# Kernel tuning notes

Hardware: AMD Instinct MI355X
Metric: run time of the kernel (lower is better)

## Reference

```python
import jax, jax.numpy as jnp
import numpy as np

# DAG: node -> list of children; node 0 is the stem output, node 6 is the cell output.
GRAPH = {1: [0], 2: [0, 1], 3: [1, 2], 4: [2, 3], 5: [3, 4], 6: [4, 5]}
OUTPUT_NODE = 6


def conv3x3(x, w, b):
    # x: [N,C,H,W], w: [O,I,3,3], b: [O]; stride 1, SAME padding (PyTorch Conv2d pad=1)
    y = jax.lax.conv_general_dilated(
        x, w, window_strides=(1, 1), padding='SAME',
        dimension_numbers=('NCHW', 'OIHW', 'NCHW'))
    return y + b[None, :, None, None]


def setup_inputs() -> dict:
    key = jax.random.key(0)
    k_x, k_w0, k_b0, k_wn, k_bn = jax.random.split(key, 5)
    scale = 0.05  # keep activations bounded through 7 stacked convs
    return {
        'x': jax.random.normal(k_x, (8, 64, 64, 64), dtype=jnp.float32),
        'W0': jax.random.normal(k_w0, (128, 64, 3, 3), dtype=jnp.float32) * scale,
        'b0': jax.random.normal(k_b0, (128,), dtype=jnp.float32) * scale,
        'Wn': jax.random.normal(k_wn, (6, 128, 128, 3, 3), dtype=jnp.float32) * scale,
        'bn': jax.random.normal(k_bn, (6, 128), dtype=jnp.float32) * scale,
    }


def reference(x, W0, b0, Wn, bn):
    # activations[0] = layers['0'](x)
    acts = {0: conv3x3(x, W0, b0)}
    # DFS with memoization over a DAG == topological evaluation of nodes 1..6.
    # Each node n sums its OWN conv (weights Wn[n-1]) applied to every child activation.
    for node in range(1, OUTPUT_NODE + 1):
        w, b = Wn[node - 1], bn[node - 1]
        out = None
        for child in GRAPH[node]:
            y = conv3x3(acts[child], w, b)
            out = y if out is None else out + y
        acts[node] = out
    return acts[OUTPUT_NODE]
```

## Files before the change

### kernel.cpp

```cpp
#include <hip/hip_runtime.h>


typedef __bf16 bf16x8 __attribute__((ext_vector_type(8)));
typedef float f32x4 __attribute__((ext_vector_type(4)));

union U4 { uint4 u; bf16x8 b; };

__device__ inline unsigned pk_bf16(float lo, float hi) {
  unsigned r;
  asm volatile("v_cvt_pk_bf16_f32 %0, %1, %2" : "=v"(r) : "v"(lo), "v"(hi));
  return r;
}

__device__ inline unsigned addpk(unsigned a, unsigned b) {
  float alo = __builtin_bit_cast(float, a << 16);
  float ahi = __builtin_bit_cast(float, a & 0xFFFF0000u);
  float blo = __builtin_bit_cast(float, b << 16);
  float bhi = __builtin_bit_cast(float, b & 0xFFFF0000u);
  return pk_bf16(alo + blo, ahi + bhi);
}

__device__ inline uint4 addpk4(uint4 a, uint4 b) {
  return make_uint4(addpk(a.x, b.x), addpk(a.y, b.y), addpk(a.z, b.z), addpk(a.w, b.w));
}

__device__ __forceinline__ void gload16(const unsigned* g, unsigned* l) {
  __builtin_amdgcn_global_load_lds(
      (const __attribute__((address_space(1))) unsigned*)(g),
      (__attribute__((address_space(3))) unsigned*)(l), 16, 0, 0);
}

template <int N>
__device__ __forceinline__ void waitcnt_vm_lgkm() {
  if constexpr (N == 0)
    asm volatile("s_waitcnt vmcnt(0) lgkmcnt(0)" ::: "memory");
  else if constexpr (N == 1)
    asm volatile("s_waitcnt vmcnt(1) lgkmcnt(0)" ::: "memory");
  else
    asm volatile("s_waitcnt vmcnt(2) lgkmcnt(0)" ::: "memory");
}

#define WB_WORDS 479232

__global__ __launch_bounds__(512) void setup_all(
    const float* __restrict__ x, const float* __restrict__ W0,
    const float* __restrict__ Wn, unsigned* __restrict__ B0,
    unsigned* __restrict__ B1, unsigned* __restrict__ B2,
    unsigned* __restrict__ T, unsigned* __restrict__ Wb) {
  __shared__ float xl[2 * 64 * 65];
  const int tid = threadIdx.x;
  const int bid = blockIdx.x;
  const int n = bid & 7;

#pragma unroll
  for (int it = 0; it < 4; ++it) {
    unsigned gid = (unsigned)bid * 512 + tid + it * 131072u;
    if (gid < WB_WORDS) {
      const float* src;
      int CIN, c, r, j;
      if (gid < 36864) {
        src = W0; CIN = 64;
        c = gid >> 11; int w = gid & 2047; r = w >> 5; j = w & 31;
      } else {
        unsigned g2 = gid - 36864;
        int s = g2 / 73728; unsigned r2 = g2 % 73728;
        src = Wn + (size_t)s * 147456; CIN = 128;
        c = r2 >> 12; int w = r2 & 4095; r = w >> 6; j = w & 63;
      }
      int ochalf = c / 9, tap = c % 9;
      int dy = tap / 3, dx = tap % 3;
      int icpair = j ^ ((r & 7) << 2);
      int oc = ochalf * 64 + r;
      size_t base = (((size_t)oc * CIN + 2 * icpair) * 3 + dy) * 3 + dx;
      Wb[gid] = pk_bf16(src[base], src[base + 9]);
    }
  }

  {
    unsigned gid = (unsigned)bid * 512 + tid;
    if (gid < 116480) {
      unsigned* buf; int CW; unsigned u;
      if (gid < 99840) {
        buf = gid < 33280 ? B0 : (gid < 66560 ? B1 : B2);
        u = gid % 33280; CW = 64;
      } else {
        buf = T; u = gid - 99840; CW = 32;
      }
      int per_n = 65 * CW;
      int nn = u / per_n;
      unsigned v = u % per_n;
      int pix = (v * 4) / CW, cw = (v * 4) % CW;
      int row, col;
      if (pix < 66) { row = 0; col = pix; }
      else if (pix < 132) { row = 65; col = pix - 66; }
      else if (pix < 196) { row = pix - 131; col = 0; }
      else { row = pix - 195; col = 65; }
      *(uint4*)&buf[((((size_t)nn * 66 + row) * 66 + col) * CW) + cw] =
          make_uint4(0, 0, 0, 0);
    }
  }

  {
    int hh = bid >> 3;
    int sub = tid >> 8;
    int t8 = tid & 255;
    int h = hh * 2 + sub;
#pragma unroll
    for (int k = 0; k < 16; ++k) {
      int idx = t8 + k * 256;
      int ic = idx >> 6, w = idx & 63;
      xl[(sub * 64 + w) * 65 + ic] = x[(((size_t)n * 64 + ic) * 64 + h) * 64 + w];
    }
    __syncthreads();
#pragma unroll
    for (int k = 0; k < 8; ++k) {
      int idx = t8 + k * 256;
      int w = idx >> 5, icp = idx & 31;
      unsigned v = pk_bf16(xl[(sub * 64 + w) * 65 + icp * 2],
                           xl[(sub * 64 + w) * 65 + icp * 2 + 1]);
      int wp = w + 1;
      int pos = icp ^ ((wp & 7) << 2);
      T[(((size_t)n * 66 + (h + 1)) * 66 + wp) * 32 + pos] = v;
    }
  }
}

template <int CIN, bool DUAL, bool OUTF32>
__global__ __launch_bounds__(512, 2) void conv_stage(
    const unsigned* __restrict__ in0, const unsigned* __restrict__ in1,
    const unsigned* __restrict__ wb, const float* __restrict__ bias,
    float bmult, void* __restrict__ outp) {
  constexpr int WPP = CIN / 2;
  constexpr int CHW = 64 * WPP;
  constexpr int WL = CHW / 2048;
  constexpr int ROWW = 66 * WPP;
  constexpr int ACTW = 6 * ROWW;
  constexpr int ALDS_W = (ACTW > 16384) ? ACTW : 16384;
  constexpr int R4_U4 = 4 * ROWW / 4;
  constexpr int R2_U4 = 2 * ROWW / 4;
  constexpr int AJ4 = (R4_U4 + 511) / 512;
  constexpr int LJ = (R2_U4 + 511) / 512;
  constexpr int KCW = CIN / 64;

  __shared__ unsigned Alds[ALDS_W];
  __shared__ unsigned Wlds[3][CHW];

  const int tid = threadIdx.x;
  const int lane = tid & 63;
  const int wav = tid >> 6;
  const int wr = wav >> 1;
  const int kh = wav & 1;
  const int l15 = lane & 15, q = lane >> 4;
  const int bid = blockIdx.x;
  const int n = bid & 7;
  const int ochalf = (bid >> 3) & 1;
  const int hq = bid >> 4;
  const int h0 = hq * 4;

  const unsigned* wbase = wb + (size_t)ochalf * 9 * CHW;
  const size_t abase = ((size_t)n * 66 + h0) * ROWW;
  const uint4* g0 = (const uint4*)(in0 + abase);
  const uint4* g1 = (const uint4*)(in1 + abase);

  uint4 l0[LJ], l1[LJ];
#pragma unroll
  for (int j = 0; j < LJ; ++j) {
    int i = tid + j * 512;
    if (i < R2_U4) {
      l0[j] = g0[R4_U4 + i];
      if (DUAL) l1[j] = g1[R4_U4 + i];
    }
  }

#pragma unroll
  for (int s = 0; s < WL; ++s)
    gload16(wbase + s * 2048 + tid * 4, &Wlds[0][s * 2048 + wav * 256]);
#pragma unroll
  for (int s = 0; s < WL; ++s)
    gload16(wbase + CHW + s * 2048 + tid * 4, &Wlds[1][s * 2048 + wav * 256]);

#pragma unroll
  for (int j = 0; j < AJ4; ++j) {
    int i = tid + j * 512;
    if (i < R4_U4) {
      uint4 v = g0[i];
      if (DUAL) v = addpk4(v, g1[i]);
      *(uint4*)&Alds[4 * i] = v;
    }
  }
  __syncthreads();

  f32x4 acc[4][4];
#pragma unroll
  for (int m = 0; m < 4; ++m)
#pragma unroll
    for (int p = 0; p < 4; ++p) acc[m][p] = (f32x4)0.f;

#pragma unroll
  for (int t = 0; t < 9; ++t) {
    if (t < 8) waitcnt_vm_lgkm<WL>();
    else waitcnt_vm_lgkm<0>();
    __builtin_amdgcn_s_barrier();
    __builtin_amdgcn_sched_barrier(0);

    const unsigned* WB = Wlds[t % 3];
    const int dy = t / 3, dx = t % 3;
    const int arow = (wr + dy) * 66;

    __builtin_amdgcn_s_setprio(1);
#pragma unroll
    for (int kc2 = 0; kc2 < KCW; ++kc2) {
      const int kc = kh * KCW + kc2;
      bf16x8 a[4];
#pragma unroll
      for (int m = 0; m < 4; ++m) {
        int r = m * 16 + l15;
        U4 u;
        u.u = *(const uint4*)&WB[r * WPP + ((kc * 16 + q * 4) ^ ((r & 7) << 2))];
        a[m] = u.b;
      }
      bf16x8 b[4];
#pragma unroll
      for (int p = 0; p < 4; ++p) {
        int col = p * 16 + l15 + dx;
        U4 u;
        u.u = *(const uint4*)&Alds[(arow + col) * WPP +
                                   ((kc * 16 + q * 4) ^ ((col & 7) << 2))];
        b[p] = u.b;
      }
#pragma unroll
      for (int m = 0; m < 4; ++m)
#pragma unroll
        for (int p = 0; p < 4; ++p)
          acc[m][p] =
              __builtin_amdgcn_mfma_f32_16x16x32_bf16(a[m], b[p], acc[m][p], 0, 0, 0);
    }
    __builtin_amdgcn_s_setprio(0);
    __builtin_amdgcn_sched_barrier(0);

    if (t == 0) {
#pragma unroll
      for (int j = 0; j < LJ; ++j) {
        int i = tid + j * 512;
        if (i < R2_U4) {
          uint4 v = l0[j];
          if (DUAL) v = addpk4(v, l1[j]);
          *(uint4*)&Alds[4 * (R4_U4 + i)] = v;
        }
      }
    }

    if (t + 2 < 9) {
#pragma unroll
      for (int s = 0; s < WL; ++s)
        gload16(wbase + (size_t)(t + 2) * CHW + s * 2048 + tid * 4,
                &Wlds[(t + 2) % 3][s * 2048 + wav * 256]);
    }
    __builtin_amdgcn_sched_barrier(0);
  }

  __syncthreads();
  float* R = (float*)Alds;
  if (kh) {
#pragma unroll
    for (int m = 0; m < 4; ++m)
#pragma unroll
      for (int p = 0; p < 4; ++p)
        *(f32x4*)&R[(wr * 16 + m * 4 + p) * 256 + lane * 4] = acc[m][p];
  }
  __syncthreads();
  if (kh) return;
#pragma unroll
  for (int m = 0; m < 4; ++m)
#pragma unroll
    for (int p = 0; p < 4; ++p) {
      f32x4 o = *(const f32x4*)&R[(wr * 16 + m * 4 + p) * 256 + lane * 4];
      acc[m][p] += o;
    }

  const int obase = ochalf * 64;
  if (OUTF32) {
    float* out = (float*)outp;
#pragma unroll
    for (int m = 0; m < 4; ++m) {
      int oc0 = obase + m * 16 + q * 4;
      float4 bb = *(const float4*)&bias[oc0];
#pragma unroll
      for (int p = 0; p < 4; ++p) {
        int w = p * 16 + l15;
#pragma unroll
        for (int j = 0; j < 4; ++j)
          out[(((size_t)n * 128 + oc0 + j) * 64 + (h0 + wr)) * 64 + w] =
              acc[m][p][j] + ((const float*)&bb)[j] * bmult;
      }
    }
  } else {
    unsigned* out = (unsigned*)outp;
#pragma unroll
    for (int m = 0; m < 4; ++m) {
      int oc0 = obase + m * 16 + q * 4;
      float4 bb = *(const float4*)&bias[oc0];
      int icp0 = oc0 >> 1;
#pragma unroll
      for (int p = 0; p < 4; ++p) {
        int w = p * 16 + l15;
        int wp = w + 1;
        unsigned lo = pk_bf16(acc[m][p][0] + bb.x * bmult, acc[m][p][1] + bb.y * bmult);
        unsigned hi = pk_bf16(acc[m][p][2] + bb.z * bmult, acc[m][p][3] + bb.w * bmult);
        int pos = icp0 ^ ((wp & 7) << 2);
        size_t base = (((size_t)n * 66 + (h0 + 1 + wr)) * 66 + wp) * 64;
        *(uint2*)&out[base + pos] = make_uint2(lo, hi);
      }
    }
  }
}

extern "C" void kernel_launch(void* const* d_in, const int* in_sizes, int n_in,
                              void* d_out, int out_size, void* d_ws,
                              size_t ws_size, hipStream_t stream) {
  const float* x = (const float*)d_in[0];
  const float* W0 = (const float*)d_in[1];
  const float* b0 = (const float*)d_in[2];
  const float* Wn = (const float*)d_in[3];
  const float* bn = (const float*)d_in[4];

  const size_t ACTB = (size_t)8 * 66 * 66 * 64;
  const size_t TW = (size_t)8 * 66 * 66 * 32;
  unsigned* B0 = (unsigned*)d_ws;
  unsigned* B1 = B0 + ACTB;
  unsigned* B2 = B1 + ACTB;
  unsigned* T = B2 + ACTB;
  unsigned* Wb = T + TW;

  setup_all<<<256, 512, 0, stream>>>(x, W0, Wn, B0, B1, B2, T, Wb);

  dim3 grid(256), blk(512);
  const unsigned* Wnode = Wb + 36864;
  const size_t NW = 73728;

  conv_stage<64, false, false><<<grid, blk, 0, stream>>>(T, T, Wb, b0, 1.f, B0);
  conv_stage<128, false, false><<<grid, blk, 0, stream>>>(B0, B0, Wnode, bn + 0, 1.f, B1);
  conv_stage<128, true, false><<<grid, blk, 0, stream>>>(B0, B1, Wnode + 1 * NW, bn + 128, 2.f, B2);
  conv_stage<128, true, false><<<grid, blk, 0, stream>>>(B1, B2, Wnode + 2 * NW, bn + 256, 2.f, B0);
  conv_stage<128, true, false><<<grid, blk, 0, stream>>>(B2, B0, Wnode + 3 * NW, bn + 384, 2.f, B1);
  conv_stage<128, true, false><<<grid, blk, 0, stream>>>(B0, B1, Wnode + 4 * NW, bn + 512, 2.f, B2);
  conv_stage<128, true, true><<<grid, blk, 0, stream>>>(B1, B2, Wnode + 5 * NW, bn + 640, 2.f, d_out);

  (void)in_sizes; (void)n_in; (void)out_size; (void)ws_size;
}
```

Measured before the change: 108.4 us.

## Retile node conv waves to 2 rows x 4 K-splits with bf16 partial reduction

```diff
diff --git a/kernel.cpp b/kernel.cpp
--- a/kernel.cpp
+++ b/kernel.cpp
@@ -38,6 +38,12 @@
     asm volatile("s_waitcnt vmcnt(1) lgkmcnt(0)" ::: "memory");
   else
     asm volatile("s_waitcnt vmcnt(2) lgkmcnt(0)" ::: "memory");
+}
+
+__device__ __forceinline__ void seal_lgkm_barrier() {
+  asm volatile("s_waitcnt lgkmcnt(0)" ::: "memory");
+  __builtin_amdgcn_s_barrier();
+  __builtin_amdgcn_sched_barrier(0);
 }
 
 #define WB_WORDS 479232
@@ -125,22 +131,13 @@
   }
 }
 
-template <int CIN, bool DUAL, bool OUTF32>
-__global__ __launch_bounds__(512, 2) void conv_stage(
-    const unsigned* __restrict__ in0, const unsigned* __restrict__ in1,
-    const unsigned* __restrict__ wb, const float* __restrict__ bias,
-    float bmult, void* __restrict__ outp) {
-  constexpr int WPP = CIN / 2;
-  constexpr int CHW = 64 * WPP;
-  constexpr int WL = CHW / 2048;
-  constexpr int ROWW = 66 * WPP;
-  constexpr int ACTW = 6 * ROWW;
-  constexpr int ALDS_W = (ACTW > 16384) ? ACTW : 16384;
-  constexpr int R4_U4 = 4 * ROWW / 4;
-  constexpr int R2_U4 = 2 * ROWW / 4;
-  constexpr int AJ4 = (R4_U4 + 511) / 512;
-  constexpr int LJ = (R2_U4 + 511) / 512;
-  constexpr int KCW = CIN / 64;
+__global__ __launch_bounds__(512, 2) void conv_stem(
+    const unsigned* __restrict__ in0, const unsigned* __restrict__ wb,
+    const float* __restrict__ bias, unsigned* __restrict__ outp) {
+  constexpr int WPP = 32, CHW = 2048, WL = 1, ROWW = 66 * 32;
+  constexpr int ACTW = 6 * ROWW, ALDS_W = 16384;
+  constexpr int R4_U4 = 4 * ROWW / 4, R2_U4 = 2 * ROWW / 4;
+  constexpr int AJ4 = (R4_U4 + 511) / 512, LJ = (R2_U4 + 511) / 512;
 
   __shared__ unsigned Alds[ALDS_W];
   __shared__ unsigned Wlds[3][CHW];
@@ -154,8 +151,147 @@
   const int bid = blockIdx.x;
   const int n = bid & 7;
   const int ochalf = (bid >> 3) & 1;
-  const int hq = bid >> 4;
-  const int h0 = hq * 4;
+  const int h0 = (bid >> 4) * 4;
+
+  const unsigned* wbase = wb + (size_t)ochalf * 9 * CHW;
+  const size_t abase = ((size_t)n * 66 + h0) * ROWW;
+  const uint4* g0 = (const uint4*)(in0 + abase);
+
+  uint4 l0[LJ];
+#pragma unroll
+  for (int j = 0; j < LJ; ++j) {
+    int i = tid + j * 512;
+    if (i < R2_U4) l0[j] = g0[R4_U4 + i];
+  }
+#pragma unroll
+  for (int j = 0; j < AJ4; ++j) {
+    int i = tid + j * 512;
+    if (i < R4_U4) *(uint4*)&Alds[4 * i] = g0[i];
+  }
+#pragma unroll
+  for (int s = 0; s < WL; ++s)
+    gload16(wbase + s * 2048 + tid * 4, &Wlds[0][s * 2048 + wav * 256]);
+#pragma unroll
+  for (int s = 0; s < WL; ++s)
+    gload16(wbase + CHW + s * 2048 + tid * 4, &Wlds[1][s * 2048 + wav * 256]);
+  seal_lgkm_barrier();
+
+  f32x4 acc[4][4];
+#pragma unroll
+  for (int m = 0; m < 4; ++m)
+#pragma unroll
+    for (int p = 0; p < 4; ++p) acc[m][p] = (f32x4)0.f;
+
+#pragma unroll
+  for (int t = 0; t < 9; ++t) {
+    if (t < 8) waitcnt_vm_lgkm<WL>();
+    else waitcnt_vm_lgkm<0>();
+    __builtin_amdgcn_s_barrier();
+    __builtin_amdgcn_sched_barrier(0);
+
+    const unsigned* WB = Wlds[t % 3];
+    const int dy = t / 3, dx = t % 3;
+    const int arow = (wr + dy) * 66;
+    const int kc = kh;
+
+    __builtin_amdgcn_s_setprio(1);
+    bf16x8 a[4];
+#pragma unroll
+    for (int m = 0; m < 4; ++m) {
+      int r = m * 16 + l15;
+      U4 u;
+      u.u = *(const uint4*)&WB[r * WPP + ((kc * 16 + q * 4) ^ ((r & 7) << 2))];
+      a[m] = u.b;
+    }
+#pragma unroll
+    for (int p = 0; p < 4; ++p) {
+      int col = p * 16 + l15 + dx;
+      U4 u;
+      u.u = *(const uint4*)&Alds[(arow + col) * WPP +
+                                 ((kc * 16 + q * 4) ^ ((col & 7) << 2))];
+      bf16x8 b = u.b;
+#pragma unroll
+      for (int m = 0; m < 4; ++m)
+        acc[m][p] = __builtin_amdgcn_mfma_f32_16x16x32_bf16(a[m], b, acc[m][p], 0, 0, 0);
+    }
+    __builtin_amdgcn_s_setprio(0);
+    __builtin_amdgcn_sched_barrier(0);
+
+    if (t == 0) {
+#pragma unroll
+      for (int j = 0; j < LJ; ++j) {
+        int i = tid + j * 512;
+        if (i < R2_U4) *(uint4*)&Alds[4 * (R4_U4 + i)] = l0[j];
+      }
+    }
+    if (t + 2 < 9) {
+#pragma unroll
+      for (int s = 0; s < WL; ++s)
+        gload16(wbase + (size_t)(t + 2) * CHW + s * 2048 + tid * 4,
+                &Wlds[(t + 2) % 3][s * 2048 + wav * 256]);
+    }
+    __builtin_amdgcn_sched_barrier(0);
+  }
+
+  __syncthreads();
+  float* R = (float*)Alds;
+  if (kh) {
+#pragma unroll
+    for (int m = 0; m < 4; ++m)
+#pragma unroll
+      for (int p = 0; p < 4; ++p)
+        *(f32x4*)&R[(wr * 16 + m * 4 + p) * 256 + lane * 4] = acc[m][p];
+  }
+  __syncthreads();
+  if (kh) return;
+#pragma unroll
+  for (int m = 0; m < 4; ++m)
+#pragma unroll
+    for (int p = 0; p < 4; ++p)
+      acc[m][p] += *(const f32x4*)&R[(wr * 16 + m * 4 + p) * 256 + lane * 4];
+
+  const int obase = ochalf * 64;
+#pragma unroll
+  for (int m = 0; m < 4; ++m) {
+    int oc0 = obase + m * 16 + q * 4;
+    float4 bb = *(const float4*)&bias[oc0];
+    int icp0 = oc0 >> 1;
+#pragma unroll
+    for (int p = 0; p < 4; ++p) {
+      int w = p * 16 + l15;
+      int wp = w + 1;
+      unsigned lo = pk_bf16(acc[m][p][0] + bb.x, acc[m][p][1] + bb.y);
+      unsigned hi = pk_bf16(acc[m][p][2] + bb.z, acc[m][p][3] + bb.w);
+      int pos = icp0 ^ ((wp & 7) << 2);
+      size_t base = (((size_t)n * 66 + (h0 + 1 + wr)) * 66 + wp) * 64;
+      *(uint2*)&outp[base + pos] = make_uint2(lo, hi);
+    }
+  }
+}
+
+template <bool DUAL, bool OUTF32>
+__global__ __launch_bounds__(512, 2) void conv_node(
+    const unsigned* __restrict__ in0, const unsigned* __restrict__ in1,
+    const unsigned* __restrict__ wb, const float* __restrict__ bias,
+    float bmult, void* __restrict__ outp) {
+  constexpr int WPP = 64, CHW = 4096, WL = 2, ROWW = 66 * 64;
+  constexpr int ACTW = 6 * ROWW;
+  constexpr int R4_U4 = 4 * ROWW / 4, R2_U4 = 2 * ROWW / 4;
+  constexpr int AJ4 = (R4_U4 + 511) / 512, LJ = (R2_U4 + 511) / 512;
+
+  __shared__ unsigned Alds[ACTW];
+  __shared__ unsigned Wlds[3][CHW];
+
+  const int tid = threadIdx.x;
+  const int lane = tid & 63;
+  const int wav = tid >> 6;
+  const int wp = wav & 1;
+  const int kh = wav >> 1;
+  const int l15 = lane & 15, q = lane >> 4;
+  const int bid = blockIdx.x;
+  const int n = bid & 7;
+  const int ochalf = (bid >> 3) & 1;
+  const int h0 = (bid >> 4) * 4;
 
   const unsigned* wbase = wb + (size_t)ochalf * 9 * CHW;
   const size_t abase = ((size_t)n * 66 + h0) * ROWW;
@@ -171,14 +307,6 @@
       if (DUAL) l1[j] = g1[R4_U4 + i];
     }
   }
-
-#pragma unroll
-  for (int s = 0; s < WL; ++s)
-    gload16(wbase + s * 2048 + tid * 4, &Wlds[0][s * 2048 + wav * 256]);
-#pragma unroll
-  for (int s = 0; s < WL; ++s)
-    gload16(wbase + CHW + s * 2048 + tid * 4, &Wlds[1][s * 2048 + wav * 256]);
-
 #pragma unroll
   for (int j = 0; j < AJ4; ++j) {
     int i = tid + j * 512;
@@ -188,13 +316,21 @@
       *(uint4*)&Alds[4 * i] = v;
     }
   }
-  __syncthreads();
-
-  f32x4 acc[4][4];
+#pragma unroll
+  for (int s = 0; s < WL; ++s)
+    gload16(wbase + s * 2048 + tid * 4, &Wlds[0][s * 2048 + wav * 256]);
+#pragma unroll
+  for (int s = 0; s < WL; ++s)
+    gload16(wbase + CHW + s * 2048 + tid * 4, &Wlds[1][s * 2048 + wav * 256]);
+  seal_lgkm_barrier();
+
+  f32x4 acc[4][8];
 #pragma unroll
   for (int m = 0; m < 4; ++m)
 #pragma unroll
-    for (int p = 0; p < 4; ++p) acc[m][p] = (f32x4)0.f;
+    for (int p = 0; p < 8; ++p) acc[m][p] = (f32x4)0.f;
+
+  const int kq = kh * 16 + q * 4;
 
 #pragma unroll
   for (int t = 0; t < 9; ++t) {
@@ -205,35 +341,27 @@
 
     const unsigned* WB = Wlds[t % 3];
     const int dy = t / 3, dx = t % 3;
-    const int arow = (wr + dy) * 66;
 
     __builtin_amdgcn_s_setprio(1);
-#pragma unroll
-    for (int kc2 = 0; kc2 < KCW; ++kc2) {
-      const int kc = kh * KCW + kc2;
-      bf16x8 a[4];
-#pragma unroll
-      for (int m = 0; m < 4; ++m) {
-        int r = m * 16 + l15;
-        U4 u;
-        u.u = *(const uint4*)&WB[r * WPP + ((kc * 16 + q * 4) ^ ((r & 7) << 2))];
-        a[m] = u.b;
-      }
-      bf16x8 b[4];
-#pragma unroll
-      for (int p = 0; p < 4; ++p) {
-        int col = p * 16 + l15 + dx;
-        U4 u;
-        u.u = *(const uint4*)&Alds[(arow + col) * WPP +
-                                   ((kc * 16 + q * 4) ^ ((col & 7) << 2))];
-        b[p] = u.b;
-      }
+    bf16x8 a[4];
+#pragma unroll
+    for (int m = 0; m < 4; ++m) {
+      int r = m * 16 + l15;
+      U4 u;
+      u.u = *(const uint4*)&WB[r * WPP + (kq ^ ((r & 7) << 2))];
+      a[m] = u.b;
+    }
+#pragma unroll
+    for (int p = 0; p < 8; ++p) {
+      int row_in = 2 * wp + (p >> 2) + dy;
+      int col = (p & 3) * 16 + l15 + dx;
+      U4 u;
+      u.u = *(const uint4*)&Alds[(row_in * 66 + col) * WPP +
+                                 (kq ^ ((col & 7) << 2))];
+      bf16x8 b = u.b;
 #pragma unroll
       for (int m = 0; m < 4; ++m)
-#pragma unroll
-        for (int p = 0; p < 4; ++p)
-          acc[m][p] =
-              __builtin_amdgcn_mfma_f32_16x16x32_bf16(a[m], b[p], acc[m][p], 0, 0, 0);
+        acc[m][p] = __builtin_amdgcn_mfma_f32_16x16x32_bf16(a[m], b, acc[m][p], 0, 0, 0);
     }
     __builtin_amdgcn_s_setprio(0);
     __builtin_amdgcn_sched_barrier(0);
@@ -249,7 +377,6 @@
         }
       }
     }
-
     if (t + 2 < 9) {
 #pragma unroll
       for (int s = 0; s < WL; ++s)
@@ -260,23 +387,34 @@
   }
 
   __syncthreads();
-  float* R = (float*)Alds;
-  if (kh) {
+  if (kh != 0) {
+    unsigned* Rb = &Alds[((kh - 1) * 2 + wp) * 4096];
 #pragma unroll
     for (int m = 0; m < 4; ++m)
 #pragma unroll
-      for (int p = 0; p < 4; ++p)
-        *(f32x4*)&R[(wr * 16 + m * 4 + p) * 256 + lane * 4] = acc[m][p];
+      for (int p = 0; p < 8; ++p) {
+        unsigned u0 = pk_bf16(acc[m][p][0], acc[m][p][1]);
+        unsigned u1 = pk_bf16(acc[m][p][2], acc[m][p][3]);
+        *(uint2*)&Rb[(m * 8 + p) * 128 + lane * 2] = make_uint2(u0, u1);
+      }
   }
   __syncthreads();
-  if (kh) return;
-#pragma unroll
-  for (int m = 0; m < 4; ++m)
-#pragma unroll
-    for (int p = 0; p < 4; ++p) {
-      f32x4 o = *(const f32x4*)&R[(wr * 16 + m * 4 + p) * 256 + lane * 4];
-      acc[m][p] += o;
-    }
+  if (kh != 0) return;
+
+#pragma unroll
+  for (int gi = 0; gi < 3; ++gi) {
+    const unsigned* Rb = &Alds[(gi * 2 + wp) * 4096];
+#pragma unroll
+    for (int m = 0; m < 4; ++m)
+#pragma unroll
+      for (int p = 0; p < 8; ++p) {
+        uint2 v = *(const uint2*)&Rb[(m * 8 + p) * 128 + lane * 2];
+        acc[m][p][0] += __builtin_bit_cast(float, v.x << 16);
+        acc[m][p][1] += __builtin_bit_cast(float, v.x & 0xFFFF0000u);
+        acc[m][p][2] += __builtin_bit_cast(float, v.y << 16);
+        acc[m][p][3] += __builtin_bit_cast(float, v.y & 0xFFFF0000u);
+      }
+  }
 
   const int obase = ochalf * 64;
   if (OUTF32) {
@@ -286,11 +424,12 @@
       int oc0 = obase + m * 16 + q * 4;
       float4 bb = *(const float4*)&bias[oc0];
 #pragma unroll
-      for (int p = 0; p < 4; ++p) {
-        int w = p * 16 + l15;
+      for (int p = 0; p < 8; ++p) {
+        int row = h0 + 2 * wp + (p >> 2);
+        int wcol = (p & 3) * 16 + l15;
 #pragma unroll
         for (int j = 0; j < 4; ++j)
-          out[(((size_t)n * 128 + oc0 + j) * 64 + (h0 + wr)) * 64 + w] =
+          out[(((size_t)n * 128 + oc0 + j) * 64 + row) * 64 + wcol] =
               acc[m][p][j] + ((const float*)&bb)[j] * bmult;
       }
     }
@@ -302,13 +441,13 @@
       float4 bb = *(const float4*)&bias[oc0];
       int icp0 = oc0 >> 1;
 #pragma unroll
-      for (int p = 0; p < 4; ++p) {
-        int w = p * 16 + l15;
-        int wp = w + 1;
+      for (int p = 0; p < 8; ++p) {
+        int row_out = h0 + 1 + 2 * wp + (p >> 2);
+        int wpad = (p & 3) * 16 + l15 + 1;
         unsigned lo = pk_bf16(acc[m][p][0] + bb.x * bmult, acc[m][p][1] + bb.y * bmult);
         unsigned hi = pk_bf16(acc[m][p][2] + bb.z * bmult, acc[m][p][3] + bb.w * bmult);
-        int pos = icp0 ^ ((wp & 7) << 2);
-        size_t base = (((size_t)n * 66 + (h0 + 1 + wr)) * 66 + wp) * 64;
+        int pos = icp0 ^ ((wpad & 7) << 2);
+        size_t base = (((size_t)n * 66 + row_out) * 66 + wpad) * 64;
         *(uint2*)&out[base + pos] = make_uint2(lo, hi);
       }
     }
@@ -338,13 +477,13 @@
   const unsigned* Wnode = Wb + 36864;
   const size_t NW = 73728;
 
-  conv_stage<64, false, false><<<grid, blk, 0, stream>>>(T, T, Wb, b0, 1.f, B0);
-  conv_stage<128, false, false><<<grid, blk, 0, stream>>>(B0, B0, Wnode, bn + 0, 1.f, B1);
-  conv_stage<128, true, false><<<grid, blk, 0, stream>>>(B0, B1, Wnode + 1 * NW, bn + 128, 2.f, B2);
-  conv_stage<128, true, false><<<grid, blk, 0, stream>>>(B1, B2, Wnode + 2 * NW, bn + 256, 2.f, B0);
-  conv_stage<128, true, false><<<grid, blk, 0, stream>>>(B2, B0, Wnode + 3 * NW, bn + 384, 2.f, B1);
-  conv_stage<128, true, false><<<grid, blk, 0, stream>>>(B0, B1, Wnode + 4 * NW, bn + 512, 2.f, B2);
-  conv_stage<128, true, true><<<grid, blk, 0, stream>>>(B1, B2, Wnode + 5 * NW, bn + 640, 2.f, d_out);
+  conv_stem<<<grid, blk, 0, stream>>>(T, Wb, b0, B0);
+  conv_node<false, false><<<grid, blk, 0, stream>>>(B0, B0, Wnode, bn + 0, 1.f, B1);
+  conv_node<true, false><<<grid, blk, 0, stream>>>(B0, B1, Wnode + 1 * NW, bn + 128, 2.f, B2);
+  conv_node<true, false><<<grid, blk, 0, stream>>>(B1, B2, Wnode + 2 * NW, bn + 256, 2.f, B0);
+  conv_node<true, false><<<grid, blk, 0, stream>>>(B2, B0, Wnode + 3 * NW, bn + 384, 2.f, B1);
+  conv_node<true, false><<<grid, blk, 0, stream>>>(B0, B1, Wnode + 4 * NW, bn + 512, 2.f, B2);
+  conv_node<true, true><<<grid, blk, 0, stream>>>(B1, B2, Wnode + 5 * NW, bn + 640, 2.f, d_out);
 
   (void)in_sizes; (void)n_in; (void)out_size; (void)ws_size;
 }
```

Measured after the change: 125.6 us. 15.9% more time.

## Precompute child-sum in producer epilogue instead of dual-loading inputs in consumer

Applied to the files above, without the earlier changes.

```diff
diff --git a/kernel.cpp b/kernel.cpp
--- a/kernel.cpp
+++ b/kernel.cpp
@@ -10,18 +10,6 @@
   unsigned r;
   asm volatile("v_cvt_pk_bf16_f32 %0, %1, %2" : "=v"(r) : "v"(lo), "v"(hi));
   return r;
-}
-
-__device__ inline unsigned addpk(unsigned a, unsigned b) {
-  float alo = __builtin_bit_cast(float, a << 16);
-  float ahi = __builtin_bit_cast(float, a & 0xFFFF0000u);
-  float blo = __builtin_bit_cast(float, b << 16);
-  float bhi = __builtin_bit_cast(float, b & 0xFFFF0000u);
-  return pk_bf16(alo + blo, ahi + bhi);
-}
-
-__device__ inline uint4 addpk4(uint4 a, uint4 b) {
-  return make_uint4(addpk(a.x, b.x), addpk(a.y, b.y), addpk(a.z, b.z), addpk(a.w, b.w));
 }
 
 __device__ __forceinline__ void gload16(const unsigned* g, unsigned* l) {
@@ -40,12 +28,18 @@
     asm volatile("s_waitcnt vmcnt(2) lgkmcnt(0)" ::: "memory");
 }
 
+__device__ __forceinline__ void seal_lgkm_barrier() {
+  asm volatile("s_waitcnt lgkmcnt(0)" ::: "memory");
+  __builtin_amdgcn_s_barrier();
+  __builtin_amdgcn_sched_barrier(0);
+}
+
 #define WB_WORDS 479232
 
 __global__ __launch_bounds__(512) void setup_all(
     const float* __restrict__ x, const float* __restrict__ W0,
-    const float* __restrict__ Wn, unsigned* __restrict__ B0,
-    unsigned* __restrict__ B1, unsigned* __restrict__ B2,
+    const float* __restrict__ Wn, unsigned* __restrict__ Aa,
+    unsigned* __restrict__ Sa, unsigned* __restrict__ Sb,
     unsigned* __restrict__ T, unsigned* __restrict__ Wb) {
   __shared__ float xl[2 * 64 * 65];
   const int tid = threadIdx.x;
@@ -81,7 +75,7 @@
     if (gid < 116480) {
       unsigned* buf; int CW; unsigned u;
       if (gid < 99840) {
-        buf = gid < 33280 ? B0 : (gid < 66560 ? B1 : B2);
+        buf = gid < 33280 ? Aa : (gid < 66560 ? Sa : Sb);
         u = gid % 33280; CW = 64;
       } else {
         buf = T; u = gid - 99840; CW = 32;
@@ -125,21 +119,20 @@
   }
 }
 
-template <int CIN, bool DUAL, bool OUTF32>
+template <int CIN, bool WRITE_S, bool WRITE_A, bool OUTF32>
 __global__ __launch_bounds__(512, 2) void conv_stage(
-    const unsigned* __restrict__ in0, const unsigned* __restrict__ in1,
+    const unsigned* __restrict__ in0, const unsigned* __restrict__ aprev,
     const unsigned* __restrict__ wb, const float* __restrict__ bias,
-    float bmult, void* __restrict__ outp) {
+    float bmult, unsigned* __restrict__ outA, unsigned* __restrict__ outS,
+    float* __restrict__ outF) {
   constexpr int WPP = CIN / 2;
   constexpr int CHW = 64 * WPP;
   constexpr int WL = CHW / 2048;
   constexpr int ROWW = 66 * WPP;
   constexpr int ACTW = 6 * ROWW;
   constexpr int ALDS_W = (ACTW > 16384) ? ACTW : 16384;
-  constexpr int R4_U4 = 4 * ROWW / 4;
-  constexpr int R2_U4 = 2 * ROWW / 4;
-  constexpr int AJ4 = (R4_U4 + 511) / 512;
-  constexpr int LJ = (R2_U4 + 511) / 512;
+  constexpr int R4_U4 = 4 * ROWW / 4, R2_U4 = 2 * ROWW / 4;
+  constexpr int AJ4 = (R4_U4 + 511) / 512, LJ = (R2_U4 + 511) / 512;
   constexpr int KCW = CIN / 64;
 
   __shared__ unsigned Alds[ALDS_W];
@@ -154,41 +147,30 @@
   const int bid = blockIdx.x;
   const int n = bid & 7;
   const int ochalf = (bid >> 3) & 1;
-  const int hq = bid >> 4;
-  const int h0 = hq * 4;
+  const int h0 = (bid >> 4) * 4;
 
   const unsigned* wbase = wb + (size_t)ochalf * 9 * CHW;
   const size_t abase = ((size_t)n * 66 + h0) * ROWW;
   const uint4* g0 = (const uint4*)(in0 + abase);
-  const uint4* g1 = (const uint4*)(in1 + abase);
-
-  uint4 l0[LJ], l1[LJ];
+
+  uint4 l0[LJ];
 #pragma unroll
   for (int j = 0; j < LJ; ++j) {
     int i = tid + j * 512;
-    if (i < R2_U4) {
-      l0[j] = g0[R4_U4 + i];
-      if (DUAL) l1[j] = g1[R4_U4 + i];
-    }
-  }
-
+    if (i < R2_U4) l0[j] = g0[R4_U4 + i];
+  }
 #pragma unroll
   for (int s = 0; s < WL; ++s)
     gload16(wbase + s * 2048 + tid * 4, &Wlds[0][s * 2048 + wav * 256]);
 #pragma unroll
   for (int s = 0; s < WL; ++s)
     gload16(wbase + CHW + s * 2048 + tid * 4, &Wlds[1][s * 2048 + wav * 256]);
-
 #pragma unroll
   for (int j = 0; j < AJ4; ++j) {
     int i = tid + j * 512;
-    if (i < R4_U4) {
-      uint4 v = g0[i];
-      if (DUAL) v = addpk4(v, g1[i]);
-      *(uint4*)&Alds[4 * i] = v;
-    }
-  }
-  __syncthreads();
+    if (i < R4_U4) *(uint4*)&Alds[4 * i] = g0[i];
+  }
+  seal_lgkm_barrier();
 
   f32x4 acc[4][4];
 #pragma unroll
@@ -203,6 +185,14 @@
     __builtin_amdgcn_s_barrier();
     __builtin_amdgcn_sched_barrier(0);
 
+    if (t + 2 < 9) {
+#pragma unroll
+      for (int s = 0; s < WL; ++s)
+        gload16(wbase + (size_t)(t + 2) * CHW + s * 2048 + tid * 4,
+                &Wlds[(t + 2) % 3][s * 2048 + wav * 256]);
+    }
+    __builtin_amdgcn_sched_barrier(0);
+
     const unsigned* WB = Wlds[t % 3];
     const int dy = t / 3, dx = t % 3;
     const int arow = (wr + dy) * 66;
@@ -219,21 +209,18 @@
         u.u = *(const uint4*)&WB[r * WPP + ((kc * 16 + q * 4) ^ ((r & 7) << 2))];
         a[m] = u.b;
       }
-      bf16x8 b[4];
 #pragma unroll
       for (int p = 0; p < 4; ++p) {
         int col = p * 16 + l15 + dx;
         U4 u;
         u.u = *(const uint4*)&Alds[(arow + col) * WPP +
                                    ((kc * 16 + q * 4) ^ ((col & 7) << 2))];
-        b[p] = u.b;
-      }
-#pragma unroll
-      for (int m = 0; m < 4; ++m)
-#pragma unroll
-        for (int p = 0; p < 4; ++p)
+        bf16x8 b = u.b;
+#pragma unroll
+        for (int m = 0; m < 4; ++m)
           acc[m][p] =
-              __builtin_amdgcn_mfma_f32_16x16x32_bf16(a[m], b[p], acc[m][p], 0, 0, 0);
+              __builtin_amdgcn_mfma_f32_16x16x32_bf16(a[m], b, acc[m][p], 0, 0, 0);
+      }
     }
     __builtin_amdgcn_s_setprio(0);
     __builtin_amdgcn_sched_barrier(0);
@@ -242,19 +229,8 @@
 #pragma unroll
       for (int j = 0; j < LJ; ++j) {
         int i = tid + j * 512;
-        if (i < R2_U4) {
-          uint4 v = l0[j];
-          if (DUAL) v = addpk4(v, l1[j]);
-          *(uint4*)&Alds[4 * (R4_U4 + i)] = v;
-        }
-      }
-    }
-
-    if (t + 2 < 9) {
-#pragma unroll
-      for (int s = 0; s < WL; ++s)
-        gload16(wbase + (size_t)(t + 2) * CHW + s * 2048 + tid * 4,
-                &Wlds[(t + 2) % 3][s * 2048 + wav * 256]);
+        if (i < R2_U4) *(uint4*)&Alds[4 * (R4_U4 + i)] = l0[j];
+      }
     }
     __builtin_amdgcn_sched_barrier(0);
   }
@@ -273,14 +249,11 @@
 #pragma unroll
   for (int m = 0; m < 4; ++m)
 #pragma unroll
-    for (int p = 0; p < 4; ++p) {
-      f32x4 o = *(const f32x4*)&R[(wr * 16 + m * 4 + p) * 256 + lane * 4];
-      acc[m][p] += o;
-    }
+    for (int p = 0; p < 4; ++p)
+      acc[m][p] += *(const f32x4*)&R[(wr * 16 + m * 4 + p) * 256 + lane * 4];
 
   const int obase = ochalf * 64;
   if (OUTF32) {
-    float* out = (float*)outp;
 #pragma unroll
     for (int m = 0; m < 4; ++m) {
       int oc0 = obase + m * 16 + q * 4;
@@ -290,12 +263,11 @@
         int w = p * 16 + l15;
 #pragma unroll
         for (int j = 0; j < 4; ++j)
-          out[(((size_t)n * 128 + oc0 + j) * 64 + (h0 + wr)) * 64 + w] =
+          outF[(((size_t)n * 128 + oc0 + j) * 64 + (h0 + wr)) * 64 + w] =
               acc[m][p][j] + ((const float*)&bb)[j] * bmult;
       }
     }
   } else {
-    unsigned* out = (unsigned*)outp;
 #pragma unroll
     for (int m = 0; m < 4; ++m) {
       int oc0 = obase + m * 16 + q * 4;
@@ -305,11 +277,22 @@
       for (int p = 0; p < 4; ++p) {
         int w = p * 16 + l15;
         int wp = w + 1;
-        unsigned lo = pk_bf16(acc[m][p][0] + bb.x * bmult, acc[m][p][1] + bb.y * bmult);
-        unsigned hi = pk_bf16(acc[m][p][2] + bb.z * bmult, acc[m][p][3] + bb.w * bmult);
         int pos = icp0 ^ ((wp & 7) << 2);
         size_t base = (((size_t)n * 66 + (h0 + 1 + wr)) * 66 + wp) * 64;
-        *(uint2*)&out[base + pos] = make_uint2(lo, hi);
+        float v0 = acc[m][p][0] + bb.x * bmult;
+        float v1 = acc[m][p][1] + bb.y * bmult;
+        float v2 = acc[m][p][2] + bb.z * bmult;
+        float v3 = acc[m][p][3] + bb.w * bmult;
+        if (WRITE_A)
+          *(uint2*)&outA[base + pos] = make_uint2(pk_bf16(v0, v1), pk_bf16(v2, v3));
+        if (WRITE_S) {
+          uint2 ap = *(const uint2*)&aprev[base + pos];
+          float s0 = v0 + __builtin_bit_cast(float, ap.x << 16);
+          float s1 = v1 + __builtin_bit_cast(float, ap.x & 0xFFFF0000u);
+          float s2 = v2 + __builtin_bit_cast(float, ap.y << 16);
+          float s3 = v3 + __builtin_bit_cast(float, ap.y & 0xFFFF0000u);
+          *(uint2*)&outS[base + pos] = make_uint2(pk_bf16(s0, s1), pk_bf16(s2, s3));
+        }
       }
     }
   }
@@ -326,25 +309,34 @@
 
   const size_t ACTB = (size_t)8 * 66 * 66 * 64;
   const size_t TW = (size_t)8 * 66 * 66 * 32;
-  unsigned* B0 = (unsigned*)d_ws;
-  unsigned* B1 = B0 + ACTB;
-  unsigned* B2 = B1 + ACTB;
-  unsigned* T = B2 + ACTB;
+  unsigned* Aa = (unsigned*)d_ws;
+  unsigned* Ab = Aa + ACTB;
+  unsigned* Sa = Ab + ACTB;
+  unsigned* Sb = Sa + ACTB;
+  unsigned* T = Sb + ACTB;
   unsigned* Wb = T + TW;
 
-  setup_all<<<256, 512, 0, stream>>>(x, W0, Wn, B0, B1, B2, T, Wb);
+  setup_all<<<256, 512, 0, stream>>>(x, W0, Wn, Aa, Sa, Sb, T, Wb);
 
   dim3 grid(256), blk(512);
-  const unsigned* Wnode = Wb + 36864;
+  const unsigned* Wd = Wb + 36864;
   const size_t NW = 73728;
-
-  conv_stage<64, false, false><<<grid, blk, 0, stream>>>(T, T, Wb, b0, 1.f, B0);
-  conv_stage<128, false, false><<<grid, blk, 0, stream>>>(B0, B0, Wnode, bn + 0, 1.f, B1);
-  conv_stage<128, true, false><<<grid, blk, 0, stream>>>(B0, B1, Wnode + 1 * NW, bn + 128, 2.f, B2);
-  conv_stage<128, true, false><<<grid, blk, 0, stream>>>(B1, B2, Wnode + 2 * NW, bn + 256, 2.f, B0);
-  conv_stage<128, true, false><<<grid, blk, 0, stream>>>(B2, B0, Wnode + 3 * NW, bn + 384, 2.f, B1);
-  conv_stage<128, true, false><<<grid, blk, 0, stream>>>(B0, B1, Wnode + 4 * NW, bn + 512, 2.f, B2);
-  conv_stage<128, true, true><<<grid, blk, 0, stream>>>(B1, B2, Wnode + 5 * NW, bn + 640, 2.f, d_out);
+  float* OF = (float*)d_out;
+
+  conv_stage<64, false, true, false><<<grid, blk, 0, stream>>>(
+      T, nullptr, Wb, b0, 1.f, Aa, nullptr, nullptr);
+  conv_stage<128, true, true, false><<<grid, blk, 0, stream>>>(
+      Aa, Aa, Wd, bn + 0, 1.f, Ab, Sa, nullptr);
+  conv_stage<128, true, true, false><<<grid, blk, 0, stream>>>(
+      Sa, Ab, Wd + 1 * NW, bn + 128, 2.f, Aa, Sb, nullptr);
+  conv_stage<128, true, true, false><<<grid, blk, 0, stream>>>(
+      Sb, Aa, Wd + 2 * NW, bn + 256, 2.f, Ab, Sa, nullptr);
+  conv_stage<128, true, true, false><<<grid, blk, 0, stream>>>(
+      Sa, Ab, Wd + 3 * NW, bn + 384, 2.f, Aa, Sb, nullptr);
+  conv_stage<128, true, false, false><<<grid, blk, 0, stream>>>(
+      Sb, Aa, Wd + 4 * NW, bn + 512, 2.f, nullptr, Sa, nullptr);
+  conv_stage<128, false, false, true><<<grid, blk, 0, stream>>>(
+      Sa, nullptr, Wd + 5 * NW, bn + 640, 2.f, nullptr, nullptr, OF);
 
   (void)in_sizes; (void)n_in; (void)out_size; (void)ws_size;
 }
```

Result: slower. 150.8 us (+39.2%).

## Load conv weights directly into registers in MFMA fragment order, drop LDS weight staging

Applied to the files above, without the earlier changes.

```diff
diff --git a/kernel.cpp b/kernel.cpp
--- a/kernel.cpp
+++ b/kernel.cpp
@@ -22,22 +22,6 @@
 
 __device__ inline uint4 addpk4(uint4 a, uint4 b) {
   return make_uint4(addpk(a.x, b.x), addpk(a.y, b.y), addpk(a.z, b.z), addpk(a.w, b.w));
-}
-
-__device__ __forceinline__ void gload16(const unsigned* g, unsigned* l) {
-  __builtin_amdgcn_global_load_lds(
-      (const __attribute__((address_space(1))) unsigned*)(g),
-      (__attribute__((address_space(3))) unsigned*)(l), 16, 0, 0);
-}
-
-template <int N>
-__device__ __forceinline__ void waitcnt_vm_lgkm() {
-  if constexpr (N == 0)
-    asm volatile("s_waitcnt vmcnt(0) lgkmcnt(0)" ::: "memory");
-  else if constexpr (N == 1)
-    asm volatile("s_waitcnt vmcnt(1) lgkmcnt(0)" ::: "memory");
-  else
-    asm volatile("s_waitcnt vmcnt(2) lgkmcnt(0)" ::: "memory");
 }
 
 #define WB_WORDS 479232
@@ -57,21 +41,26 @@
     unsigned gid = (unsigned)bid * 512 + tid + it * 131072u;
     if (gid < WB_WORDS) {
       const float* src;
-      int CIN, c, r, j;
+      int CIN, c, w;
       if (gid < 36864) {
         src = W0; CIN = 64;
-        c = gid >> 11; int w = gid & 2047; r = w >> 5; j = w & 31;
+        c = gid >> 11; w = gid & 2047;
       } else {
         unsigned g2 = gid - 36864;
         int s = g2 / 73728; unsigned r2 = g2 % 73728;
         src = Wn + (size_t)s * 147456; CIN = 128;
-        c = r2 >> 12; int w = r2 & 4095; r = w >> 6; j = w & 63;
-      }
-      int ochalf = c / 9, tap = c % 9;
+        c = r2 >> 12; w = r2 & 4095;
+      }
+      int och = c / 9, tap = c % 9;
       int dy = tap / 3, dx = tap % 3;
-      int icpair = j ^ ((r & 7) << 2);
-      int oc = ochalf * 64 + r;
-      size_t base = (((size_t)oc * CIN + 2 * icpair) * 3 + dy) * 3 + dx;
+      int f = w >> 8;
+      int nkc = CIN / 32;
+      int m = f / nkc, kc = f % nkc;
+      int r8 = w & 255;
+      int lane = r8 >> 2, wq = r8 & 3;
+      int oc = och * 64 + m * 16 + (lane & 15);
+      int icp = kc * 16 + (lane >> 4) * 4 + wq;
+      size_t base = (((size_t)oc * CIN + 2 * icp) * 3 + dy) * 3 + dx;
       Wb[gid] = pk_bf16(src[base], src[base + 9]);
     }
   }
@@ -132,18 +121,16 @@
     float bmult, void* __restrict__ outp) {
   constexpr int WPP = CIN / 2;
   constexpr int CHW = 64 * WPP;
-  constexpr int WL = CHW / 2048;
+  constexpr int CH_U4 = CHW / 4;
+  constexpr int NKC_TOT = WPP / 16;
+  constexpr int KCW = NKC_TOT / 2;
   constexpr int ROWW = 66 * WPP;
   constexpr int ACTW = 6 * ROWW;
   constexpr int ALDS_W = (ACTW > 16384) ? ACTW : 16384;
-  constexpr int R4_U4 = 4 * ROWW / 4;
-  constexpr int R2_U4 = 2 * ROWW / 4;
-  constexpr int AJ4 = (R4_U4 + 511) / 512;
-  constexpr int LJ = (R2_U4 + 511) / 512;
-  constexpr int KCW = CIN / 64;
+  constexpr int ACT_U4 = ACTW / 4;
+  constexpr int AJ = (ACT_U4 + 511) / 512;
 
   __shared__ unsigned Alds[ALDS_W];
-  __shared__ unsigned Wlds[3][CHW];
 
   const int tid = threadIdx.x;
   const int lane = tid & 63;
@@ -154,40 +141,32 @@
   const int bid = blockIdx.x;
   const int n = bid & 7;
   const int ochalf = (bid >> 3) & 1;
-  const int hq = bid >> 4;
-  const int h0 = hq * 4;
-
-  const unsigned* wbase = wb + (size_t)ochalf * 9 * CHW;
-  const size_t abase = ((size_t)n * 66 + h0) * ROWW;
-  const uint4* g0 = (const uint4*)(in0 + abase);
-  const uint4* g1 = (const uint4*)(in1 + abase);
-
-  uint4 l0[LJ], l1[LJ];
-#pragma unroll
-  for (int j = 0; j < LJ; ++j) {
-    int i = tid + j * 512;
-    if (i < R2_U4) {
-      l0[j] = g0[R4_U4 + i];
-      if (DUAL) l1[j] = g1[R4_U4 + i];
-    }
-  }
-
-#pragma unroll
-  for (int s = 0; s < WL; ++s)
-    gload16(wbase + s * 2048 + tid * 4, &Wlds[0][s * 2048 + wav * 256]);
-#pragma unroll
-  for (int s = 0; s < WL; ++s)
-    gload16(wbase + CHW + s * 2048 + tid * 4, &Wlds[1][s * 2048 + wav * 256]);
-
-#pragma unroll
-  for (int j = 0; j < AJ4; ++j) {
-    int i = tid + j * 512;
-    if (i < R4_U4) {
-      uint4 v = g0[i];
-      if (DUAL) v = addpk4(v, g1[i]);
-      *(uint4*)&Alds[4 * i] = v;
-    }
-  }
+  const int h0 = (bid >> 4) * 4;
+
+  const uint4* wg = (const uint4*)(wb + (size_t)ochalf * 9 * CHW);
+
+  {
+    const size_t abase = ((size_t)n * 66 + h0) * ROWW;
+    const uint4* g0 = (const uint4*)(in0 + abase);
+    const uint4* g1 = (const uint4*)(in1 + abase);
+#pragma unroll
+    for (int j = 0; j < AJ; ++j) {
+      int i = tid + j * 512;
+      if (i < ACT_U4) {
+        uint4 v = g0[i];
+        if (DUAL) v = addpk4(v, g1[i]);
+        *(uint4*)&Alds[4 * i] = v;
+      }
+    }
+  }
+
+  uint4 wcur[4][KCW], wnxt[4][KCW];
+#pragma unroll
+  for (int m = 0; m < 4; ++m)
+#pragma unroll
+    for (int kc2 = 0; kc2 < KCW; ++kc2)
+      wcur[m][kc2] = wg[(m * NKC_TOT + kh * KCW + kc2) * 64 + lane];
+
   __syncthreads();
 
   f32x4 acc[4][4];
@@ -198,12 +177,15 @@
 
 #pragma unroll
   for (int t = 0; t < 9; ++t) {
-    if (t < 8) waitcnt_vm_lgkm<WL>();
-    else waitcnt_vm_lgkm<0>();
-    __builtin_amdgcn_s_barrier();
-    __builtin_amdgcn_sched_barrier(0);
-
-    const unsigned* WB = Wlds[t % 3];
+    if (t < 8) {
+#pragma unroll
+      for (int m = 0; m < 4; ++m)
+#pragma unroll
+        for (int kc2 = 0; kc2 < KCW; ++kc2)
+          wnxt[m][kc2] =
+              wg[(t + 1) * CH_U4 + (m * NKC_TOT + kh * KCW + kc2) * 64 + lane];
+    }
+
     const int dy = t / 3, dx = t % 3;
     const int arow = (wr + dy) * 66;
 
@@ -214,49 +196,27 @@
       bf16x8 a[4];
 #pragma unroll
       for (int m = 0; m < 4; ++m) {
-        int r = m * 16 + l15;
-        U4 u;
-        u.u = *(const uint4*)&WB[r * WPP + ((kc * 16 + q * 4) ^ ((r & 7) << 2))];
-        a[m] = u.b;
-      }
-      bf16x8 b[4];
+        U4 u; u.u = wcur[m][kc2]; a[m] = u.b;
+      }
 #pragma unroll
       for (int p = 0; p < 4; ++p) {
         int col = p * 16 + l15 + dx;
         U4 u;
         u.u = *(const uint4*)&Alds[(arow + col) * WPP +
                                    ((kc * 16 + q * 4) ^ ((col & 7) << 2))];
-        b[p] = u.b;
-      }
-#pragma unroll
-      for (int m = 0; m < 4; ++m)
-#pragma unroll
-        for (int p = 0; p < 4; ++p)
+        bf16x8 b = u.b;
+#pragma unroll
+        for (int m = 0; m < 4; ++m)
           acc[m][p] =
-              __builtin_amdgcn_mfma_f32_16x16x32_bf16(a[m], b[p], acc[m][p], 0, 0, 0);
+              __builtin_amdgcn_mfma_f32_16x16x32_bf16(a[m], b, acc[m][p], 0, 0, 0);
+      }
     }
     __builtin_amdgcn_s_setprio(0);
-    __builtin_amdgcn_sched_barrier(0);
-
-    if (t == 0) {
-#pragma unroll
-      for (int j = 0; j < LJ; ++j) {
-        int i = tid + j * 512;
-        if (i < R2_U4) {
-          uint4 v = l0[j];
-          if (DUAL) v = addpk4(v, l1[j]);
-          *(uint4*)&Alds[4 * (R4_U4 + i)] = v;
-        }
-      }
-    }
-
-    if (t + 2 < 9) {
-#pragma unroll
-      for (int s = 0; s < WL; ++s)
-        gload16(wbase + (size_t)(t + 2) * CHW + s * 2048 + tid * 4,
-                &Wlds[(t + 2) % 3][s * 2048 + wav * 256]);
-    }
-    __builtin_amdgcn_sched_barrier(0);
+
+#pragma unroll
+    for (int m = 0; m < 4; ++m)
+#pragma unroll
+      for (int kc2 = 0; kc2 < KCW; ++kc2) wcur[m][kc2] = wnxt[m][kc2];
   }
 
   __syncthreads();
@@ -273,10 +233,8 @@
 #pragma unroll
   for (int m = 0; m < 4; ++m)
 #pragma unroll
-    for (int p = 0; p < 4; ++p) {
-      f32x4 o = *(const f32x4*)&R[(wr * 16 + m * 4 + p) * 256 + lane * 4];
-      acc[m][p] += o;
-    }
+    for (int p = 0; p < 4; ++p)
+      acc[m][p] += *(const f32x4*)&R[(wr * 16 + m * 4 + p) * 256 + lane * 4];
 
   const int obase = ochalf * 64;
   if (OUTF32) {
```

After: 107.7 us. Within noise of the previous version (-0.6%).
